# Performance work log

Hardware: AMD Instinct MI355X
Metric: run time of the kernel (lower is better)

Reference implementation:

```python
import jax, jax.numpy as jnp
import numpy as np

# Device / physics constants for group_idx = 0 (from the original source)
V_REF = 0.25
G_MIN = 1.0 / 983.3
G_MAX = 1.0 / 281.3
N_AVG = 2.132
N_STD = 0.095

BATCH, N_IN, N_OUT = 256, 784, 512


def setup_inputs() -> dict:
    key = jax.random.key(0)
    k1, k2, k3, k4, k5, k6 = jax.random.split(key, 6)
    stdv = 1.0 / np.sqrt(N_IN)
    x = jax.random.normal(k1, (BATCH, N_IN), dtype=jnp.float32)
    # weights initialized N(0.5, stdv) as in build()
    w_pos = 0.5 + stdv * jax.random.normal(k2, (N_IN, N_OUT), dtype=jnp.float32)
    w_neg = 0.5 + stdv * jax.random.normal(k3, (N_IN, N_OUT), dtype=jnp.float32)
    b_pos = 0.5 * jnp.ones((N_OUT,), dtype=jnp.float32)
    b_neg = 0.5 * jnp.ones((N_OUT,), dtype=jnp.float32)
    # per-device IV nonlinearity samples n ~ N(n_avg, n_std), shape = G shape
    n_param = N_AVG + N_STD * jax.random.normal(k6, (N_IN + 1, 2 * N_OUT), dtype=jnp.float32)
    return {"x": x, "w_pos": w_pos, "w_neg": w_neg, "b_pos": b_pos,
            "b_neg": b_neg, "n_param": n_param}


def _memristor_dense(x, w_pos, w_neg, b_pos, b_neg, n_param):
    # Fold biases in as an extra crossbar row, interleave pos/neg columns.
    cw_pos = jnp.concatenate([w_pos, b_pos[None, :]], axis=0)   # (n_in+1, n_out)
    cw_neg = jnp.concatenate([w_neg, b_neg[None, :]], axis=0)
    weights = jnp.stack([cw_pos, cw_neg], axis=-1)              # (n_in+1, n_out, 2)
    weights = weights.reshape(cw_pos.shape[0], -1)              # (n_in+1, 2*n_out) interleaved
    inputs = jnp.concatenate(
        [x, jnp.ones((x.shape[0], 1), dtype=x.dtype)], axis=1)  # (batch, n_in+1)

    max_weight = jnp.max(jnp.abs(weights))
    k_G = (G_MAX - G_MIN) / max_weight
    # weight params -> conductances (params are nonnegative by construction)
    G = G_MIN + k_G * jnp.clip(weights, 0.0, None)              # (n_in+1, 2*n_out)

    k_V = 2.0 * V_REF
    V = k_V * inputs                                            # (batch, n_in+1)

    # Nonlinear IV: I = sign(V) * V_ref * G * (|V|/V_ref)^log2(n)
    exponent = jnp.log2(n_param)                                # (n_in+1, 2*n_out)
    ratio = jnp.abs(V) / V_REF                                  # (batch, n_in+1)
    I_ind = (jnp.sign(V)[:, :, None] * V_REF * G[None, :, :]
             * ratio[:, :, None] ** exponent[None, :, :])       # (batch, n_in+1, 2*n_out)
    I = jnp.sum(I_ind, axis=1)                                  # (batch, 2*n_out)

    # Currents -> outputs: differential pairs, undo V and G scaling
    I_total = I[:, 0::2] - I[:, 1::2]                           # (batch, n_out)
    y = I_total / (k_V * k_G)
    return y


def reference(x, w_pos, w_neg, b_pos, b_neg, n_param):
    return _memristor_dense(x, w_pos, w_neg, b_pos, b_neg, n_param)
```

## Files before the change

### kernel.cpp

```cpp
#include <hip/hip_runtime.h>

#define NIN   784
#define NOUT  512
#define NROWS 785
#define BATCH 256
#define CHUNK 25
#define LSPAD 33

static constexpr float G_MIN_F  = (float)(1.0 / 983.3);
static constexpr float G_DIFF_F = (float)(1.0 / 281.3 - 1.0 / 983.3);

__device__ __forceinline__ float dlog2(float v) { return __builtin_amdgcn_logf(v); }
__device__ __forceinline__ float dexp2(float v) { return __builtin_amdgcn_exp2f(v); }

#define WS_PART_OFF 256
#define WS_TAB_OFF  4096

__global__ __launch_bounds__(256) void mk_max(
    const float* __restrict__ wp, const float* __restrict__ wn,
    const float* __restrict__ bp, const float* __restrict__ bn,
    float* __restrict__ part, float4* __restrict__ out4)
{
    const int gid = blockIdx.x * 256 + threadIdx.x;
    out4[gid] = make_float4(0.f, 0.f, 0.f, 0.f);

    float m = 0.0f;
    const int n4 = NIN * NOUT / 4;
    const float4* wp4 = (const float4*)wp;
    const float4* wn4 = (const float4*)wn;
    for (int idx = gid; idx < n4; idx += gridDim.x * 256) {
        float4 a = wp4[idx], b = wn4[idx];
        m = fmaxf(m, fmaxf(fmaxf(fabsf(a.x), fabsf(a.y)), fmaxf(fabsf(a.z), fabsf(a.w))));
        m = fmaxf(m, fmaxf(fmaxf(fabsf(b.x), fabsf(b.y)), fmaxf(fabsf(b.z), fabsf(b.w))));
    }
    if (blockIdx.x == 0 && threadIdx.x < NOUT) {
        m = fmaxf(m, fabsf(bp[threadIdx.x]));
        m = fmaxf(m, fabsf(bn[threadIdx.x]));
    }
    #pragma unroll
    for (int off = 1; off < 64; off <<= 1)
        m = fmaxf(m, __shfl_xor(m, off, 64));
    __shared__ float sm[4];
    if ((threadIdx.x & 63) == 0) sm[threadIdx.x >> 6] = m;
    __syncthreads();
    if (threadIdx.x == 0)
        part[blockIdx.x] = fmaxf(fmaxf(sm[0], sm[1]), fmaxf(sm[2], sm[3]));
}

__global__ __launch_bounds__(128) void mk_kg(
    const float* __restrict__ part, float* __restrict__ kg)
{
    float m = part[threadIdx.x];
    #pragma unroll
    for (int off = 1; off < 64; off <<= 1)
        m = fmaxf(m, __shfl_xor(m, off, 64));
    __shared__ float sm[2];
    if ((threadIdx.x & 63) == 0) sm[threadIdx.x >> 6] = m;
    __syncthreads();
    if (threadIdx.x == 0) {
        m = fmaxf(sm[0], sm[1]);
        const float kG = G_DIFF_F / m;
        kg[0] = kG;
        kg[1] = 0.5f / kG;
    }
}

__global__ __launch_bounds__(256) void mk_table(
    const float* __restrict__ wp, const float* __restrict__ wn,
    const float* __restrict__ bp, const float* __restrict__ bn,
    const float* __restrict__ npar, const float* __restrict__ kg,
    float4* __restrict__ tab)
{
    const int t = blockIdx.x * 256 + threadIdx.x;
    if (t >= NROWS * NOUT) return;
    const int i = t >> 9, jp = t & 511;
    const float kG = kg[0];
    float wpv, wnv;
    if (i < NIN) { wpv = wp[i * NOUT + jp]; wnv = wn[i * NOUT + jp]; }
    else         { wpv = bp[jp];            wnv = bn[jp]; }
    const float2 nv = *(const float2*)(&npar[i * (2 * NOUT) + 2 * jp]);
    float4 r;
    r.x = dlog2(nv.x);
    r.y = dlog2(fmaf(kG, fmaxf(wpv, 0.0f), G_MIN_F));
    r.z = dlog2(nv.y);
    r.w = dlog2(fmaf(kG, fmaxf(wnv, 0.0f), G_MIN_F));
    tab[t] = r;
}

__global__ __launch_bounds__(256) void mk_main(
    const float* __restrict__ x, const float4* __restrict__ tab,
    const float* __restrict__ kg, float* __restrict__ out)
{
    const int tx = threadIdx.x & 63;
    const int ty = threadIdx.x >> 6;
    const int jp = blockIdx.x * 64 + tx;
    const int b0 = blockIdx.y * 32;
    const int i0 = blockIdx.z * CHUNK;
    const int iN = min(NROWS - i0, CHUNK);

    __shared__ float2 Ls[CHUNK * LSPAD];
    for (int t = threadIdx.x; t < 32 * 32; t += 256) {
        const int bb = t >> 5, ii = t & 31;
        if (ii < iN) {
            const int i = i0 + ii;
            const float v = (i < NIN) ? x[(b0 + bb) * NIN + i] : 1.0f;
            const float s = (v > 0.0f) ? 1.0f : ((v < 0.0f) ? -1.0f : 0.0f);
            Ls[ii * LSPAD + bb] = make_float2(dlog2(2.0f * fabsf(v)), s);
        }
    }
    __syncthreads();

    float acc[8];
    #pragma unroll
    for (int b = 0; b < 8; ++b) acc[b] = 0.0f;

    const float4* trow = &tab[i0 * NOUT + jp];

#define STEP(ii)                                                          \
    {                                                                     \
        const float4 tv = trow[(ii) * NOUT];                              \
        const float2* lsrow = &Ls[(ii) * LSPAD + ty * 8];                 \
        _Pragma("unroll")                                                 \
        for (int b = 0; b < 8; ++b) {                                     \
            const float2 ls = lsrow[b];                                   \
            const float tp = dexp2(fmaf(tv.x, ls.x, tv.y));               \
            const float tn = dexp2(fmaf(tv.z, ls.x, tv.w));               \
            acc[b] = fmaf(ls.y, tp - tn, acc[b]);                         \
        }                                                                 \
    }

    if (iN == CHUNK) {
        #pragma unroll 5
        for (int ii = 0; ii < CHUNK; ++ii) STEP(ii);
    } else {
        for (int ii = 0; ii < iN; ++ii) STEP(ii);
    }
#undef STEP

    const float C = kg[1];
    #pragma unroll
    for (int b = 0; b < 8; ++b)
        unsafeAtomicAdd(&out[(b0 + ty * 8 + b) * NOUT + jp], C * acc[b]);
}

__global__ __launch_bounds__(256) void mk_main_fb(
    const float* __restrict__ x,  const float* __restrict__ wp,
    const float* __restrict__ wn, const float* __restrict__ bp,
    const float* __restrict__ bn, const float* __restrict__ npar,
    const float* __restrict__ kg, float* __restrict__ out)
{
    const int tx = threadIdx.x & 63;
    const int ty = threadIdx.x >> 6;
    const int jp = blockIdx.x * 64 + tx;
    const int b0 = blockIdx.y * 32;
    const int i0 = blockIdx.z * CHUNK;
    const int iN = min(NROWS - i0, CHUNK);

    __shared__ float2 Ls[CHUNK * LSPAD];
    for (int t = threadIdx.x; t < 32 * 32; t += 256) {
        const int bb = t >> 5, ii = t & 31;
        if (ii < iN) {
            const int i = i0 + ii;
            const float v = (i < NIN) ? x[(b0 + bb) * NIN + i] : 1.0f;
            const float s = (v > 0.0f) ? 1.0f : ((v < 0.0f) ? -1.0f : 0.0f);
            Ls[ii * LSPAD + bb] = make_float2(dlog2(2.0f * fabsf(v)), s);
        }
    }
    __syncthreads();

    const float kG = kg[0];
    float acc[8];
    #pragma unroll
    for (int b = 0; b < 8; ++b) acc[b] = 0.0f;

    for (int ii = 0; ii < iN; ++ii) {
        const int i = i0 + ii;
        float wpv, wnv;
        if (i < NIN) { wpv = wp[i * NOUT + jp]; wnv = wn[i * NOUT + jp]; }
        else         { wpv = bp[jp];            wnv = bn[jp]; }
        const float2 nv = *(const float2*)(&npar[i * (2 * NOUT) + 2 * jp]);
        const float lgGp = dlog2(fmaf(kG, fmaxf(wpv, 0.0f), G_MIN_F));
        const float lgGn = dlog2(fmaf(kG, fmaxf(wnv, 0.0f), G_MIN_F));
        const float ep = dlog2(nv.x);
        const float en = dlog2(nv.y);
        const float2* lsrow = &Ls[ii * LSPAD + ty * 8];
        #pragma unroll
        for (int b = 0; b < 8; ++b) {
            const float2 ls = lsrow[b];
            const float tp = dexp2(fmaf(ep, ls.x, lgGp));
            const float tn = dexp2(fmaf(en, ls.x, lgGn));
            acc[b] = fmaf(ls.y, tp - tn, acc[b]);
        }
    }

    const float C = kg[1];
    #pragma unroll
    for (int b = 0; b < 8; ++b)
        unsafeAtomicAdd(&out[(b0 + ty * 8 + b) * NOUT + jp], C * acc[b]);
}

extern "C" void kernel_launch(void* const* d_in, const int* in_sizes, int n_in,
                              void* d_out, int out_size, void* d_ws, size_t ws_size,
                              hipStream_t stream) {
    const float* x    = (const float*)d_in[0];
    const float* wp   = (const float*)d_in[1];
    const float* wn   = (const float*)d_in[2];
    const float* bp   = (const float*)d_in[3];
    const float* bn   = (const float*)d_in[4];
    const float* npar = (const float*)d_in[5];
    float*        out = (float*)d_out;
    float*         kg = (float*)d_ws;
    float*       part = (float*)((char*)d_ws + WS_PART_OFF);

    mk_max<<<128, 256, 0, stream>>>(wp, wn, bp, bn, part, (float4*)out);
    mk_kg<<<1, 128, 0, stream>>>(part, kg);

    const size_t tab_bytes = (size_t)NROWS * NOUT * sizeof(float4);
    dim3 grid(8, 8, 32);
    if (ws_size >= WS_TAB_OFF + tab_bytes) {
        float4* tab = (float4*)((char*)d_ws + WS_TAB_OFF);
        mk_table<<<(NROWS * NOUT + 255) / 256, 256, 0, stream>>>(
            wp, wn, bp, bn, npar, kg, tab);
        mk_main<<<grid, 256, 0, stream>>>(x, tab, kg, out);
    } else {
        mk_main_fb<<<grid, 256, 0, stream>>>(x, wp, wn, bp, bn, npar, kg, out);
    }
}
```

Baseline: 43.36 us.

## Replace atomic accumulation with per-chunk partials and a separate reduce kernel

The main kernel now writes each K-chunk's partial sums to a workspace buffer instead of doing float atomics into the output, and a new reduce kernel sums the 32 partials and applies the scale. The mk_kg kernel is removed by having the table and reduce kernels recompute the max from the 128 partial maxima. The table is padded to 800 rows so the main loop has no tail branch. This trades atomic contention and one launch for an extra 16 MB partial write and read plus a reduce launch.

```diff
diff --git a/kernel.cpp b/kernel.cpp
--- a/kernel.cpp
+++ b/kernel.cpp
@@ -3,9 +3,11 @@
 #define NIN   784
 #define NOUT  512
 #define NROWS 785
+#define NPAD  800
 #define BATCH 256
 #define CHUNK 25
 #define LSPAD 33
+#define NZ    32
 
 static constexpr float G_MIN_F  = (float)(1.0 / 983.3);
 static constexpr float G_DIFF_F = (float)(1.0 / 281.3 - 1.0 / 983.3);
@@ -13,17 +15,29 @@
 __device__ __forceinline__ float dlog2(float v) { return __builtin_amdgcn_logf(v); }
 __device__ __forceinline__ float dexp2(float v) { return __builtin_amdgcn_exp2f(v); }
 
-#define WS_PART_OFF 256
+#define WS_PM_OFF   0
+#define WS_KG_OFF   2048
 #define WS_TAB_OFF  4096
+#define WS_PART_OFF (WS_TAB_OFF + (size_t)NPAD * NOUT * 16)
+#define WS_TOTAL    (WS_PART_OFF + (size_t)NZ * BATCH * NOUT * 4)
+
+__device__ __forceinline__ float load_maxw(const float* __restrict__ pm, int tid) {
+    float m = pm[tid & 127];
+    #pragma unroll
+    for (int off = 1; off < 64; off <<= 1)
+        m = fmaxf(m, __shfl_xor(m, off, 64));
+    __shared__ float sm2[4];
+    if ((tid & 63) == 0) sm2[tid >> 6] = m;
+    __syncthreads();
+    return fmaxf(fmaxf(sm2[0], sm2[1]), fmaxf(sm2[2], sm2[3]));
+}
 
 __global__ __launch_bounds__(256) void mk_max(
     const float* __restrict__ wp, const float* __restrict__ wn,
     const float* __restrict__ bp, const float* __restrict__ bn,
-    float* __restrict__ part, float4* __restrict__ out4)
+    float* __restrict__ part)
 {
     const int gid = blockIdx.x * 256 + threadIdx.x;
-    out4[gid] = make_float4(0.f, 0.f, 0.f, 0.f);
-
     float m = 0.0f;
     const int n4 = NIN * NOUT / 4;
     const float4* wp4 = (const float4*)wp;
@@ -47,6 +61,94 @@
         part[blockIdx.x] = fmaxf(fmaxf(sm[0], sm[1]), fmaxf(sm[2], sm[3]));
 }
 
+__global__ __launch_bounds__(256) void mk_table(
+    const float* __restrict__ wp, const float* __restrict__ wn,
+    const float* __restrict__ bp, const float* __restrict__ bn,
+    const float* __restrict__ npar, const float* __restrict__ pm,
+    float4* __restrict__ tab)
+{
+    const int tid = threadIdx.x;
+    const float kG = G_DIFF_F / load_maxw(pm, tid);
+    const int t = blockIdx.x * 256 + tid;
+    const int i = t >> 9, jp = t & 511;
+    float4 r = make_float4(0.f, 0.f, 0.f, 0.f);
+    if (i < NROWS) {
+        float wpv, wnv;
+        if (i < NIN) { wpv = wp[i * NOUT + jp]; wnv = wn[i * NOUT + jp]; }
+        else         { wpv = bp[jp];            wnv = bn[jp]; }
+        const float2 nv = *(const float2*)(&npar[i * (2 * NOUT) + 2 * jp]);
+        r.x = dlog2(nv.x);
+        r.y = dlog2(fmaf(kG, fmaxf(wpv, 0.0f), G_MIN_F));
+        r.z = dlog2(nv.y);
+        r.w = dlog2(fmaf(kG, fmaxf(wnv, 0.0f), G_MIN_F));
+    }
+    tab[t] = r;
+}
+
+__global__ __launch_bounds__(256) void mk_main(
+    const float* __restrict__ x, const float4* __restrict__ tab,
+    float* __restrict__ part)
+{
+    const int tx = threadIdx.x & 63;
+    const int ty = threadIdx.x >> 6;
+    const int jp = blockIdx.x * 64 + tx;
+    const int b0 = blockIdx.y * 32;
+    const int i0 = blockIdx.z * CHUNK;
+
+    __shared__ float2 Ls[CHUNK * LSPAD];
+    for (int t = threadIdx.x; t < 32 * 32; t += 256) {
+        const int bb = t >> 5, ii = t & 31;
+        if (ii < CHUNK) {
+            const int i = i0 + ii;
+            float L = 0.0f, s = 0.0f;
+            if (i < NIN) {
+                const float v = x[(b0 + bb) * NIN + i];
+                s = (v > 0.0f) ? 1.0f : ((v < 0.0f) ? -1.0f : 0.0f);
+                L = dlog2(2.0f * fabsf(v));
+            } else if (i == NIN) { L = 1.0f; s = 1.0f; }
+            Ls[ii * LSPAD + bb] = make_float2(L, s);
+        }
+    }
+    __syncthreads();
+
+    float acc[8];
+    #pragma unroll
+    for (int b = 0; b < 8; ++b) acc[b] = 0.0f;
+
+    const float4* trow = &tab[i0 * NOUT + jp];
+    #pragma unroll 5
+    for (int ii = 0; ii < CHUNK; ++ii) {
+        const float4 tv = trow[ii * NOUT];
+        const float2* lsrow = &Ls[ii * LSPAD + ty * 8];
+        #pragma unroll
+        for (int b = 0; b < 8; ++b) {
+            const float2 ls = lsrow[b];
+            const float tp = dexp2(fmaf(tv.x, ls.x, tv.y));
+            const float tn = dexp2(fmaf(tv.z, ls.x, tv.w));
+            acc[b] = fmaf(ls.y, tp - tn, acc[b]);
+        }
+    }
+
+    float* pr = &part[(size_t)blockIdx.z * (BATCH * NOUT) + b0 * NOUT + jp];
+    #pragma unroll
+    for (int b = 0; b < 8; ++b)
+        pr[(ty * 8 + b) * NOUT] = acc[b];
+}
+
+__global__ __launch_bounds__(256) void mk_reduce(
+    const float* __restrict__ part, const float* __restrict__ pm,
+    float* __restrict__ out)
+{
+    const int tid = threadIdx.x;
+    const float C = 0.5f * load_maxw(pm, tid) / G_DIFF_F;
+    const int g = blockIdx.x * 256 + tid;
+    float s = 0.0f;
+    #pragma unroll
+    for (int z = 0; z < NZ; ++z)
+        s += part[(size_t)z * (BATCH * NOUT) + g];
+    out[g] = C * s;
+}
+
 __global__ __launch_bounds__(128) void mk_kg(
     const float* __restrict__ part, float* __restrict__ kg)
 {
@@ -65,82 +167,9 @@
     }
 }
 
-__global__ __launch_bounds__(256) void mk_table(
-    const float* __restrict__ wp, const float* __restrict__ wn,
-    const float* __restrict__ bp, const float* __restrict__ bn,
-    const float* __restrict__ npar, const float* __restrict__ kg,
-    float4* __restrict__ tab)
-{
-    const int t = blockIdx.x * 256 + threadIdx.x;
-    if (t >= NROWS * NOUT) return;
-    const int i = t >> 9, jp = t & 511;
-    const float kG = kg[0];
-    float wpv, wnv;
-    if (i < NIN) { wpv = wp[i * NOUT + jp]; wnv = wn[i * NOUT + jp]; }
-    else         { wpv = bp[jp];            wnv = bn[jp]; }
-    const float2 nv = *(const float2*)(&npar[i * (2 * NOUT) + 2 * jp]);
-    float4 r;
-    r.x = dlog2(nv.x);
-    r.y = dlog2(fmaf(kG, fmaxf(wpv, 0.0f), G_MIN_F));
-    r.z = dlog2(nv.y);
-    r.w = dlog2(fmaf(kG, fmaxf(wnv, 0.0f), G_MIN_F));
-    tab[t] = r;
-}
-
-__global__ __launch_bounds__(256) void mk_main(
-    const float* __restrict__ x, const float4* __restrict__ tab,
-    const float* __restrict__ kg, float* __restrict__ out)
-{
-    const int tx = threadIdx.x & 63;
-    const int ty = threadIdx.x >> 6;
-    const int jp = blockIdx.x * 64 + tx;
-    const int b0 = blockIdx.y * 32;
-    const int i0 = blockIdx.z * CHUNK;
-    const int iN = min(NROWS - i0, CHUNK);
-
-    __shared__ float2 Ls[CHUNK * LSPAD];
-    for (int t = threadIdx.x; t < 32 * 32; t += 256) {
-        const int bb = t >> 5, ii = t & 31;
-        if (ii < iN) {
-            const int i = i0 + ii;
-            const float v = (i < NIN) ? x[(b0 + bb) * NIN + i] : 1.0f;
-            const float s = (v > 0.0f) ? 1.0f : ((v < 0.0f) ? -1.0f : 0.0f);
-            Ls[ii * LSPAD + bb] = make_float2(dlog2(2.0f * fabsf(v)), s);
-        }
-    }
-    __syncthreads();
-
-    float acc[8];
-    #pragma unroll
-    for (int b = 0; b < 8; ++b) acc[b] = 0.0f;
-
-    const float4* trow = &tab[i0 * NOUT + jp];
-
-#define STEP(ii)                                                          \
-    {                                                                     \
-        const float4 tv = trow[(ii) * NOUT];                              \
-        const float2* lsrow = &Ls[(ii) * LSPAD + ty * 8];                 \
-        _Pragma("unroll")                                                 \
-        for (int b = 0; b < 8; ++b) {                                     \
-            const float2 ls = lsrow[b];                                   \
-            const float tp = dexp2(fmaf(tv.x, ls.x, tv.y));               \
-            const float tn = dexp2(fmaf(tv.z, ls.x, tv.w));               \
-            acc[b] = fmaf(ls.y, tp - tn, acc[b]);                         \
-        }                                                                 \
-    }
-
-    if (iN == CHUNK) {
-        #pragma unroll 5
-        for (int ii = 0; ii < CHUNK; ++ii) STEP(ii);
-    } else {
-        for (int ii = 0; ii < iN; ++ii) STEP(ii);
-    }
-#undef STEP
-
-    const float C = kg[1];
-    #pragma unroll
-    for (int b = 0; b < 8; ++b)
-        unsafeAtomicAdd(&out[(b0 + ty * 8 + b) * NOUT + jp], C * acc[b]);
+__global__ __launch_bounds__(256) void mk_zero(float4* __restrict__ out4)
+{
+    out4[blockIdx.x * 256 + threadIdx.x] = make_float4(0.f, 0.f, 0.f, 0.f);
 }
 
 __global__ __launch_bounds__(256) void mk_main_fb(
@@ -209,20 +238,21 @@
     const float* bn   = (const float*)d_in[4];
     const float* npar = (const float*)d_in[5];
     float*        out = (float*)d_out;
-    float*         kg = (float*)d_ws;
-    float*       part = (float*)((char*)d_ws + WS_PART_OFF);
-
-    mk_max<<<128, 256, 0, stream>>>(wp, wn, bp, bn, part, (float4*)out);
-    mk_kg<<<1, 128, 0, stream>>>(part, kg);
-
-    const size_t tab_bytes = (size_t)NROWS * NOUT * sizeof(float4);
-    dim3 grid(8, 8, 32);
-    if (ws_size >= WS_TAB_OFF + tab_bytes) {
-        float4* tab = (float4*)((char*)d_ws + WS_TAB_OFF);
-        mk_table<<<(NROWS * NOUT + 255) / 256, 256, 0, stream>>>(
-            wp, wn, bp, bn, npar, kg, tab);
-        mk_main<<<grid, 256, 0, stream>>>(x, tab, kg, out);
+    float*         pm = (float*)((char*)d_ws + WS_PM_OFF);
+
+    mk_max<<<128, 256, 0, stream>>>(wp, wn, bp, bn, pm);
+
+    dim3 grid(8, 8, NZ);
+    if (ws_size >= WS_TOTAL) {
+        float4* tab  = (float4*)((char*)d_ws + WS_TAB_OFF);
+        float*  part = (float*)((char*)d_ws + WS_PART_OFF);
+        mk_table<<<NPAD * NOUT / 256, 256, 0, stream>>>(wp, wn, bp, bn, npar, pm, tab);
+        mk_main<<<grid, 256, 0, stream>>>(x, tab, part);
+        mk_reduce<<<BATCH * NOUT / 256, 256, 0, stream>>>(part, pm, out);
     } else {
+        float* kg = (float*)((char*)d_ws + WS_KG_OFF);
+        mk_kg<<<1, 128, 0, stream>>>(pm, kg);
+        mk_zero<<<BATCH * NOUT / 4 / 256, 256, 0, stream>>>((float4*)out);
         mk_main_fb<<<grid, 256, 0, stream>>>(x, wp, wn, bp, bn, npar, kg, out);
     }
 }
```

After: 48.90 us. +12.8%, slower.
